# Optimization experiments

Hardware: AMD Instinct MI355X
Metric: run time of the kernel (lower is better)

## Reference

```python
import jax, jax.numpy as jnp
import numpy as np

B, D, DC, K = 65536, 768, 192, 100  # batch patterns, hidden_dim, codebook_hidden, num_clusters
LN_EPS = 1e-5


def setup_inputs() -> dict:
    key = jax.random.key(0)
    ks = jax.random.split(key, 12)
    w = lambda k, shape: (jax.random.normal(k, shape, jnp.float32) * 0.02)
    return {
        "hidden": jax.random.normal(ks[0], (B, D), jnp.float32),
        "W_low": w(ks[1], (DC, D)),   # nn.Linear(hidden_dim, codebook_hidden), torch (out,in)
        "b_low": jnp.zeros((DC,), jnp.float32),
        "ln_g": jnp.ones((DC,), jnp.float32),
        "ln_b": jnp.zeros((DC,), jnp.float32),
        "Wq": w(ks[2], (DC, DC)),
        "Wk": w(ks[3], (DC, DC)),
        "Wv": w(ks[4], (DC, DC)),
        "Wo": w(ks[5], (DC, DC)),
        "codebook": w(ks[6], (K, DC)),  # vp_codebook.weight
        "W_high": w(ks[7], (D, DC)),    # nn.Linear(codebook_hidden, hidden_dim)
        "b_high": jnp.zeros((D,), jnp.float32),
    }


def reference(hidden, W_low, b_low, ln_g, ln_b, Wq, Wk, Wv, Wo, codebook, W_high, b_high):
    # low projection: 768 -> 192
    pat = hidden @ W_low.T + b_low  # [B, DC]
    # LayerNorm over last dim
    mu = jnp.mean(pat, axis=-1, keepdims=True)
    var = jnp.mean(jnp.square(pat - mu), axis=-1, keepdims=True)
    pat = (pat - mu) * jax.lax.rsqrt(var + LN_EPS) * ln_g + ln_b
    # CrossAttention against codebook with NEGATED scores (distance-like)
    q = pat @ Wq.T            # [B, DC]
    k = codebook @ Wk.T       # [K, DC]
    v = codebook @ Wv.T       # [K, DC]
    scores = -(q @ k.T)       # [B, K]
    attn_w = jax.nn.softmax(scores, axis=-1)
    attn_out = (attn_w @ v) @ Wo.T  # [B, DC]
    # argmin over attention weights -> codebook selection + gather
    idx = jnp.argmin(attn_w, axis=-1)   # [B] int
    z_q = codebook[idx]                 # [B, DC]
    # high projection on both branches
    pat_h = attn_out @ W_high.T + b_high  # [B, D]
    zq_h = z_q @ W_high.T + b_high        # [B, D]
    # straight-through estimator: pat + (z_q - pat).detach()
    return pat_h + jax.lax.stop_gradient(zq_h - pat_h)
```

## Files before the change

kernel.cpp:

```cpp
#include <hip/hip_runtime.h>

#define NB    65536
#define DIN   768
#define DCB   192
#define KCL   100
#define NJ    112

#define OFF_S    0
#define OFF_CS   19200
#define OFF_U    19312
#define OFF_T    19424
#define OFF_ZH   19536
#define OFF_FLAG 96336
#define OFF_CNT  96337
#define OFF_MTH  96340
#define OFF_KTIL 96340
#define OFF_LIST 139348

#define MARGIN 1e-4f
#define MTSC   64.0f
#define SCINV  0.015625f

typedef __attribute__((ext_vector_type(8))) _Float16 half8;
typedef __attribute__((ext_vector_type(4))) float    f32x4;


__global__ void kA1(const float* __restrict__ cb, const float* __restrict__ Wk,
                    float* __restrict__ ktil, int* __restrict__ flag,
                    int* __restrict__ cnt) {
  __shared__ float cbrow[DCB];
  int j = blockIdx.x, i = threadIdx.x;
  if (j == 0 && i == 0) { *flag = 0; *cnt = 0; }
  cbrow[i] = cb[j*DCB + i];
  __syncthreads();
  const float4* wr = (const float4*)&Wk[(size_t)i * DCB];
  double s0 = 0.0, s1 = 0.0;
  #pragma unroll 4
  for (int m4 = 0; m4 < DCB/4; m4++) {
    float4 w = wr[m4];
    s0 += (double)w.x * (double)cbrow[m4*4+0] + (double)w.z * (double)cbrow[m4*4+2];
    s1 += (double)w.y * (double)cbrow[m4*4+1] + (double)w.w * (double)cbrow[m4*4+3];
  }
  ktil[j*DCB+i] = (float)(s0 + s1);
}

__global__ void kA2(const float* __restrict__ Wq, const float* __restrict__ ktil,
                    const float* __restrict__ ln_g, const float* __restrict__ ln_b,
                    const float* __restrict__ b_low,
                    float* __restrict__ S, float* __restrict__ csum,
                    float* __restrict__ tv, float* __restrict__ u,
                    int* __restrict__ flag) {
  __shared__ float krow[DCB];
  __shared__ double red[DCB];
  int j = blockIdx.x, c = threadIdx.x;
  krow[c] = ktil[j*DCB + c];
  __syncthreads();
  double a0 = 0.0, a1 = 0.0;
  #pragma unroll 4
  for (int i = 0; i < DCB; i += 2) {
    a0 += (double)Wq[i*DCB+c]     * (double)krow[i];
    a1 += (double)Wq[(i+1)*DCB+c] * (double)krow[i+1];
  }
  double a = a0 + a1;
  float Sv = ln_g[c] * (float)a;
  S[j*DCB+c] = Sv;

  red[c] = (double)Sv; __syncthreads();
  if (c == 0) {
    double p0=0,p1=0,p2=0,p3=0;
    for (int i = 0; i < DCB; i += 4) { p0+=red[i]; p1+=red[i+1]; p2+=red[i+2]; p3+=red[i+3]; }
    csum[j] = (float)(p0+p1+p2+p3);
  }
  __syncthreads();
  red[c] = (double)ln_b[c] * a; __syncthreads();
  if (c == 0) {
    double p0=0,p1=0,p2=0,p3=0;
    for (int i = 0; i < DCB; i += 4) { p0+=red[i]; p1+=red[i+1]; p2+=red[i+2]; p3+=red[i+3]; }
    float tf = (float)(p0+p1+p2+p3); tv[j] = tf;
    if (tf != 0.0f) atomicOr(flag, 1);
  }
  __syncthreads();
  red[c] = (double)b_low[c] * (double)Sv; __syncthreads();
  if (c == 0) {
    double p0=0,p1=0,p2=0,p3=0;
    for (int i = 0; i < DCB; i += 4) { p0+=red[i]; p1+=red[i+1]; p2+=red[i+2]; p3+=red[i+3]; }
    u[j] = (float)(p0+p1+p2+p3);
  }
  __syncthreads();
  if (j == 0) {
    red[c] = (double)b_low[c]; __syncthreads();
    if (c == 0) {
      double p0=0,p1=0,p2=0,p3=0;
      for (int i = 0; i < DCB; i += 4) { p0+=red[i]; p1+=red[i+1]; p2+=red[i+2]; p3+=red[i+3]; }
      u[KCL] = (float)((p0+p1+p2+p3) / (double)DCB);
      for (int p = KCL+1; p < NJ; p++) u[p] = 0.f;
      for (int p = KCL;   p < NJ; p++) { csum[p] = 0.f; tv[p] = 0.f; }
    }
  }
}

__global__ void kA3(const float* __restrict__ W_low, const float* __restrict__ S,
                    _Float16* __restrict__ Mth) {
  __shared__ float srow[DCB];
  int j = blockIdx.x / 3, st = blockIdx.x % 3;
  int t = threadIdx.x;
  int d = st * 256 + t;
  if (j < KCL && t < DCB) srow[t] = S[j*DCB + t];
  __syncthreads();
  float v;
  if (j < KCL) {
    double a = 0.0;
    for (int c = 0; c < DCB; c++) a += (double)W_low[(size_t)c*DIN + d] * (double)srow[c];
    v = (float)a;
  } else if (j == KCL) {
    double a = 0.0;
    for (int c = 0; c < DCB; c++) a += (double)W_low[(size_t)c*DIN + d];
    v = (float)(a / (double)DCB);
  } else {
    v = 0.f;
  }
  Mth[(size_t)j*DIN + d] = (_Float16)(v * MTSC);
}

__global__ void kA4(const float* __restrict__ cb, const float* __restrict__ W_high,
                    const float* __restrict__ b_high, float* __restrict__ ZH) {
  __shared__ float cbrow[DCB];
  int j = blockIdx.x, t = threadIdx.x;
  if (t < DCB) cbrow[t] = cb[j*DCB + t];
  __syncthreads();
  #pragma unroll
  for (int kd = 0; kd < 3; kd++) {
    int d = t + 256*kd;
    const float4* wr = (const float4*)&W_high[(size_t)d * DCB];
    double s0 = 0.0, s1 = 0.0;
    #pragma unroll 4
    for (int c4 = 0; c4 < DCB/4; c4++) {
      float4 w = wr[c4];
      s0 += (double)w.x * (double)cbrow[c4*4+0] + (double)w.z * (double)cbrow[c4*4+2];
      s1 += (double)w.y * (double)cbrow[c4*4+1] + (double)w.w * (double)cbrow[c4*4+3];
    }
    ZH[(size_t)j*DIN + d] = (float)(s0 + s1 + (double)b_high[d]);
  }
}

__global__ __launch_bounds__(256, 2)
void kB(const float* __restrict__ hidden, float* __restrict__ out,
        const _Float16* __restrict__ Mth, const float* __restrict__ u,
        const float* __restrict__ csum, const float* __restrict__ ZH,
        const int* __restrict__ flag, int* __restrict__ cnt,
        unsigned short* __restrict__ list,
        const float* __restrict__ S, const float* __restrict__ tv,
        const float* __restrict__ W_low, const float* __restrict__ b_low) {
  const int tid = threadIdx.x;
  __shared__ __align__(16) _Float16 Bs[2][14336];
  if (*flag == 0) {
    const int lane = tid & 63;
    const int wv   = tid >> 6;
    const int lj   = lane & 15, lk = lane >> 4;
    const int R    = blockIdx.x * 128 + wv * 32;

    char* BsB = (char*)&Bs[0][0];

    const char* srcp[7]; int dstp[7];
    #pragma unroll
    for (int i = 0; i < 7; i++) {
      int o    = ((wv*7 + i)*64 + lane) * 16;
      int row  = o >> 8;
      int colb = o & 255;
      srcp[i] = (const char*)Mth + row*1536 + colb;
      dstp[i] = row*256 + (colb ^ ((row & 7) << 4));
    }

    const float* A0 = hidden + (size_t)(R + lj) * DIN + lk * 8;
    const float* A1 = A0 + 16 * DIN;

    f32x4 acc[2][7];
    #pragma unroll
    for (int m = 0; m < 2; m++)
      #pragma unroll
      for (int nj = 0; nj < 7; nj++) acc[m][nj] = (f32x4){0.f, 0.f, 0.f, 0.f};

    uint4 stg[7];
    #pragma unroll
    for (int i = 0; i < 7; i++) stg[i] = *(const uint4*)(srcp[i]);
    float4 Ac[2][2];
    Ac[0][0] = *(const float4*)(A0); Ac[0][1] = *(const float4*)(A0 + 4);
    Ac[1][0] = *(const float4*)(A1); Ac[1][1] = *(const float4*)(A1 + 4);
    #pragma unroll
    for (int i = 0; i < 7; i++) *(uint4*)(BsB + dstp[i]) = stg[i];
    __syncthreads();

    for (int kc = 0; kc < 6; kc++) {
      const int cur = kc & 1;
      if (kc < 5) {
        #pragma unroll
        for (int i = 0; i < 7; i++)
          stg[i] = *(const uint4*)(srcp[i] + (kc + 1) * 256);
      }
      #pragma unroll
      for (int s = 0; s < 4; s++) {
        const int g = kc*4 + s;
        float4 An[2][2];
        if (g < 23) {
          const float* p0 = A0 + (g + 1) * 32;
          const float* p1 = A1 + (g + 1) * 32;
          An[0][0] = *(const float4*)(p0); An[0][1] = *(const float4*)(p0 + 4);
          An[1][0] = *(const float4*)(p1); An[1][1] = *(const float4*)(p1 + 4);
        }
        half8 bfr[7];
        const char* bbase = BsB + cur * 28672;
        #pragma unroll
        for (int nj = 0; nj < 7; nj++) {
          int row = nj*16 + lj;
          int off = row*256 + ((lk*16 + s*64) ^ ((row & 7) << 4));
          bfr[nj] = *(const half8*)(bbase + off);
        }
        #pragma unroll
        for (int m = 0; m < 2; m++) {
          half8 ah;
          ah[0] = (_Float16)Ac[m][0].x; ah[1] = (_Float16)Ac[m][0].y;
          ah[2] = (_Float16)Ac[m][0].z; ah[3] = (_Float16)Ac[m][0].w;
          ah[4] = (_Float16)Ac[m][1].x; ah[5] = (_Float16)Ac[m][1].y;
          ah[6] = (_Float16)Ac[m][1].z; ah[7] = (_Float16)Ac[m][1].w;
          #pragma unroll
          for (int nj = 0; nj < 7; nj++)
            acc[m][nj] = __builtin_amdgcn_mfma_f32_16x16x32_f16(ah, bfr[nj], acc[m][nj], 0, 0, 0);
        }
        if (g < 23) {
          Ac[0][0] = An[0][0]; Ac[0][1] = An[0][1];
          Ac[1][0] = An[1][0]; Ac[1][1] = An[1][1];
        }
      }
      if (kc < 5) {
        #pragma unroll
        for (int i = 0; i < 7; i++)
          *(uint4*)(BsB + (cur ^ 1) * 28672 + dstp[i]) = stg[i];
      }
      __syncthreads();
    }

    float uj[7], cj[7];
    #pragma unroll
    for (int nj = 0; nj < 7; nj++) { int j = nj*16 + lj; uj[nj] = u[j]; cj[nj] = csum[j]; }
    const float u100 = u[KCL];

    int idxr[2][4];
    #pragma unroll
    for (int m = 0; m < 2; m++) {
      #pragma unroll
      for (int r = 0; r < 4; r++) {
        float mu = __shfl(acc[m][6][r], (lane & 48) + 4, 64) * SCINV + u100;
        float b1 = -3.4e38f, b2 = -3.4e38f; int i1 = 0;
        #pragma unroll
        for (int nj = 0; nj < 7; nj++) {
          int j = nj*16 + lj;
          float sv = acc[m][nj][r] * SCINV + uj[nj] - mu * cj[nj];
          sv = (j < KCL) ? sv : -3.4e38f;
          if (sv > b1) { b2 = b1; b1 = sv; i1 = j; }
          else if (sv > b2) { b2 = sv; }
        }
        #pragma unroll
        for (int off = 1; off < 16; off <<= 1) {
          float ob1 = __shfl_xor(b1, off, 64);
          int   oi1 = __shfl_xor(i1, off, 64);
          float ob2 = __shfl_xor(b2, off, 64);
          if (ob1 > b1 || (ob1 == b1 && oi1 < i1)) {
            b2 = fmaxf(b1, fmaxf(b2, ob2)); b1 = ob1; i1 = oi1;
          } else {
            b2 = fmaxf(ob1, fmaxf(b2, ob2));
          }
        }
        idxr[m][r] = i1;
        if (lj == 0 && (b1 - b2) <= MARGIN) {
          int p = atomicAdd(cnt, 1);
          list[p] = (unsigned short)(R + m*16 + lk*4 + r);
        }
      }
    }

    #pragma unroll
    for (int rr = 0; rr < 32; rr++) {
      int idx = __shfl(idxr[rr >> 4][rr & 3], ((rr & 15) >> 2) << 4, 64);
      const float4* zs = (const float4*)(ZH + (size_t)idx * DIN);
      float4* od = (float4*)(out + (size_t)(R + rr) * DIN);
      od[lane]       = zs[lane];
      od[lane + 64]  = zs[lane + 64];
      od[lane + 128] = zs[lane + 128];
    }
  } else {
    __shared__ float hrow2[DIN];
    __shared__ float patv[DCB];
    __shared__ float redf[2];
    __shared__ float Gsc[KCL];
    __shared__ int   sidx;
    const int r0 = blockIdx.x * 128;
    for (int rr = 0; rr < 128; rr++) {
      const size_t row = (size_t)(r0 + rr);
      __syncthreads();
      for (int d = tid; d < DIN; d += 256) hrow2[d] = hidden[row * DIN + d];
      __syncthreads();
      if (tid < DCB) {
        float a = b_low[tid];
        for (int d = 0; d < DIN; d++) a += hrow2[d] * W_low[(size_t)tid * DIN + d];
        patv[tid] = a;
      }
      __syncthreads();
      if (tid == 0) {
        float mu = 0.f; for (int c = 0; c < DCB; c++) mu += patv[c]; mu /= (float)DCB;
        float var = 0.f; for (int c = 0; c < DCB; c++) { float dd = patv[c] - mu; var += dd * dd; }
        var /= (float)DCB;
        redf[0] = mu; redf[1] = rsqrtf(var + 1e-5f);
      }
      __syncthreads();
      if (tid < DCB) patv[tid] = (patv[tid] - redf[0]) * redf[1];
      __syncthreads();
      if (tid < KCL) {
        float s = tv[tid];
        for (int c = 0; c < DCB; c++) s += patv[c] * S[(size_t)tid * DCB + c];
        Gsc[tid] = s;
      }
      __syncthreads();
      if (tid == 0) {
        float best = -3.4e38f; int bi = 0;
        for (int j = 0; j < KCL; j++) if (Gsc[j] > best) { best = Gsc[j]; bi = j; }
        sidx = bi;
      }
      __syncthreads();
      {
        int idx = sidx;
        for (int d4 = tid; d4 < DIN / 4; d4 += 256) {
          float4 v = *(const float4*)&ZH[(size_t)idx * DIN + d4 * 4];
          *(float4*)&out[row * DIN + d4 * 4] = v;
        }
      }
    }
  }
}

__global__ void kC(const float* __restrict__ hidden, float* __restrict__ out,
                   const float* __restrict__ W_low, const float* __restrict__ b_low,
                   const float* __restrict__ S, const float* __restrict__ ZH,
                   const int* __restrict__ cnt, const unsigned short* __restrict__ list) {
  __shared__ float  hrow[DIN];
  __shared__ double pat[DCB];
  __shared__ double smu;
  __shared__ double sc[KCL];
  __shared__ int    bidx;
  const int n = *cnt;
  const int tid = threadIdx.x;
  for (int it = blockIdx.x; it < n; it += gridDim.x) {
    const int row = (int)list[it];
    __syncthreads();
    for (int d = tid; d < DIN; d += 256) hrow[d] = hidden[(size_t)row * DIN + d];
    __syncthreads();
    if (tid < DCB) {
      const float* wl = W_low + (size_t)tid * DIN;
      double a = (double)b_low[tid];
      for (int d = 0; d < DIN; d += 4) {
        a += (double)hrow[d]   * (double)wl[d]
           + (double)hrow[d+1] * (double)wl[d+1]
           + (double)hrow[d+2] * (double)wl[d+2]
           + (double)hrow[d+3] * (double)wl[d+3];
      }
      pat[tid] = a;
    }
    __syncthreads();
    if (tid == 0) {
      double m = 0.0;
      for (int c = 0; c < DCB; c++) m += pat[c];
      smu = m / (double)DCB;
    }
    __syncthreads();
    if (tid < KCL) {
      const float* sr = S + (size_t)tid * DCB;
      const double mu = smu;
      double a = 0.0;
      for (int c = 0; c < DCB; c++) a += (pat[c] - mu) * (double)sr[c];
      sc[tid] = a;
    }
    __syncthreads();
    if (tid == 0) {
      double best = -1e300; int bi = 0;
      for (int j = 0; j < KCL; j++)
        if (sc[j] > best) { best = sc[j]; bi = j; }
      bidx = bi;
    }
    __syncthreads();
    {
      const int idx = bidx;
      for (int d4 = tid; d4 < DIN / 4; d4 += 256) {
        float4 v = *(const float4*)(ZH + (size_t)idx * DIN + d4 * 4);
        *(float4*)(out + (size_t)row * DIN + d4 * 4) = v;
      }
    }
  }
}

extern "C" void kernel_launch(void* const* d_in, const int* in_sizes, int n_in,
                              void* d_out, int out_size, void* d_ws, size_t ws_size,
                              hipStream_t stream) {
  const float* hidden = (const float*)d_in[0];
  const float* W_low  = (const float*)d_in[1];
  const float* b_low  = (const float*)d_in[2];
  const float* ln_g   = (const float*)d_in[3];
  const float* ln_b   = (const float*)d_in[4];
  const float* Wq     = (const float*)d_in[5];
  const float* Wk     = (const float*)d_in[6];
  const float* cb     = (const float*)d_in[9];
  const float* W_high = (const float*)d_in[10];
  const float* b_high = (const float*)d_in[11];
  float* out = (float*)d_out;
  float* ws  = (float*)d_ws;

  float*          S    = ws + OFF_S;
  float*          csum = ws + OFF_CS;
  float*          u    = ws + OFF_U;
  float*          tv   = ws + OFF_T;
  float*          ZH   = ws + OFF_ZH;
  int*            flag = (int*)(ws + OFF_FLAG);
  int*            cnt  = (int*)(ws + OFF_CNT);
  _Float16*       Mth  = (_Float16*)(ws + OFF_MTH);
  float*          ktil = ws + OFF_KTIL;
  unsigned short* list = (unsigned short*)(ws + OFF_LIST);

  kA1<<<KCL, DCB, 0, stream>>>(cb, Wk, ktil, flag, cnt);
  kA2<<<KCL, DCB, 0, stream>>>(Wq, ktil, ln_g, ln_b, b_low, S, csum, tv, u, flag);
  kA3<<<NJ*3, 256, 0, stream>>>(W_low, S, Mth);
  kA4<<<KCL, 256, 0, stream>>>(cb, W_high, b_high, ZH);
  kB<<<NB / 128, 256, 0, stream>>>(hidden, out, Mth, u, csum, ZH, flag, cnt, list,
                                   S, tv, W_low, b_low);
  kC<<<2048, 256, 0, stream>>>(hidden, out, W_low, b_low, S, ZH, cnt, list);
}
```

Baseline: 577.7 us.

## Fuse precompute kernels into one launch and batch fallback rows in kC

Merges the four small precompute kernels (K projection, S/csum/u computation, Mth build, ZH build) into one kernel whose blocks take different roles, and zeroes the flag/count with a memset instead of doing it inside a kernel. This removes launch overhead and the serial dependencies between the small kernels. The fallback kernel kC now processes 8 listed rows per block, so each W_low and S value it loads is reused across 8 rows. The cost is more shared memory and registers per block, and a long serial chain inside the fused precompute blocks.

```diff
diff --git a/kernel.cpp b/kernel.cpp
--- a/kernel.cpp
+++ b/kernel.cpp
@@ -14,7 +14,6 @@
 #define OFF_FLAG 96336
 #define OFF_CNT  96337
 #define OFF_MTH  96340
-#define OFF_KTIL 96340
 #define OFF_LIST 139348
 
 #define MARGIN 1e-4f
@@ -24,122 +23,130 @@
 typedef __attribute__((ext_vector_type(8))) _Float16 half8;
 typedef __attribute__((ext_vector_type(4))) float    f32x4;
 
-
-__global__ void kA1(const float* __restrict__ cb, const float* __restrict__ Wk,
-                    float* __restrict__ ktil, int* __restrict__ flag,
-                    int* __restrict__ cnt) {
-  __shared__ float cbrow[DCB];
-  int j = blockIdx.x, i = threadIdx.x;
-  if (j == 0 && i == 0) { *flag = 0; *cnt = 0; }
-  cbrow[i] = cb[j*DCB + i];
-  __syncthreads();
-  const float4* wr = (const float4*)&Wk[(size_t)i * DCB];
-  double s0 = 0.0, s1 = 0.0;
-  #pragma unroll 4
-  for (int m4 = 0; m4 < DCB/4; m4++) {
-    float4 w = wr[m4];
-    s0 += (double)w.x * (double)cbrow[m4*4+0] + (double)w.z * (double)cbrow[m4*4+2];
-    s1 += (double)w.y * (double)cbrow[m4*4+1] + (double)w.w * (double)cbrow[m4*4+3];
-  }
-  ktil[j*DCB+i] = (float)(s0 + s1);
-}
-
-__global__ void kA2(const float* __restrict__ Wq, const float* __restrict__ ktil,
-                    const float* __restrict__ ln_g, const float* __restrict__ ln_b,
-                    const float* __restrict__ b_low,
-                    float* __restrict__ S, float* __restrict__ csum,
-                    float* __restrict__ tv, float* __restrict__ u,
-                    int* __restrict__ flag) {
-  __shared__ float krow[DCB];
-  __shared__ double red[DCB];
-  int j = blockIdx.x, c = threadIdx.x;
-  krow[c] = ktil[j*DCB + c];
-  __syncthreads();
-  double a0 = 0.0, a1 = 0.0;
-  #pragma unroll 4
-  for (int i = 0; i < DCB; i += 2) {
-    a0 += (double)Wq[i*DCB+c]     * (double)krow[i];
-    a1 += (double)Wq[(i+1)*DCB+c] * (double)krow[i+1];
-  }
-  double a = a0 + a1;
-  float Sv = ln_g[c] * (float)a;
-  S[j*DCB+c] = Sv;
-
-  red[c] = (double)Sv; __syncthreads();
-  if (c == 0) {
-    double p0=0,p1=0,p2=0,p3=0;
-    for (int i = 0; i < DCB; i += 4) { p0+=red[i]; p1+=red[i+1]; p2+=red[i+2]; p3+=red[i+3]; }
-    csum[j] = (float)(p0+p1+p2+p3);
-  }
-  __syncthreads();
-  red[c] = (double)ln_b[c] * a; __syncthreads();
-  if (c == 0) {
-    double p0=0,p1=0,p2=0,p3=0;
-    for (int i = 0; i < DCB; i += 4) { p0+=red[i]; p1+=red[i+1]; p2+=red[i+2]; p3+=red[i+3]; }
-    float tf = (float)(p0+p1+p2+p3); tv[j] = tf;
-    if (tf != 0.0f) atomicOr(flag, 1);
-  }
-  __syncthreads();
-  red[c] = (double)b_low[c] * (double)Sv; __syncthreads();
-  if (c == 0) {
-    double p0=0,p1=0,p2=0,p3=0;
-    for (int i = 0; i < DCB; i += 4) { p0+=red[i]; p1+=red[i+1]; p2+=red[i+2]; p3+=red[i+3]; }
-    u[j] = (float)(p0+p1+p2+p3);
-  }
-  __syncthreads();
-  if (j == 0) {
-    red[c] = (double)b_low[c]; __syncthreads();
-    if (c == 0) {
-      double p0=0,p1=0,p2=0,p3=0;
-      for (int i = 0; i < DCB; i += 4) { p0+=red[i]; p1+=red[i+1]; p2+=red[i+2]; p3+=red[i+3]; }
-      u[KCL] = (float)((p0+p1+p2+p3) / (double)DCB);
-      for (int p = KCL+1; p < NJ; p++) u[p] = 0.f;
-      for (int p = KCL;   p < NJ; p++) { csum[p] = 0.f; tv[p] = 0.f; }
-    }
-  }
-}
-
-__global__ void kA3(const float* __restrict__ W_low, const float* __restrict__ S,
-                    _Float16* __restrict__ Mth) {
-  __shared__ float srow[DCB];
-  int j = blockIdx.x / 3, st = blockIdx.x % 3;
-  int t = threadIdx.x;
-  int d = st * 256 + t;
-  if (j < KCL && t < DCB) srow[t] = S[j*DCB + t];
-  __syncthreads();
-  float v;
-  if (j < KCL) {
-    double a = 0.0;
-    for (int c = 0; c < DCB; c++) a += (double)W_low[(size_t)c*DIN + d] * (double)srow[c];
-    v = (float)a;
-  } else if (j == KCL) {
-    double a = 0.0;
-    for (int c = 0; c < DCB; c++) a += (double)W_low[(size_t)c*DIN + d];
-    v = (float)(a / (double)DCB);
+__global__ void kA(const float* __restrict__ cb, const float* __restrict__ Wk,
+                   const float* __restrict__ Wq, const float* __restrict__ ln_g,
+                   const float* __restrict__ ln_b, const float* __restrict__ b_low,
+                   const float* __restrict__ W_low, const float* __restrict__ W_high,
+                   const float* __restrict__ b_high,
+                   float* __restrict__ S, float* __restrict__ csum,
+                   float* __restrict__ tv, float* __restrict__ u,
+                   _Float16* __restrict__ Mth, float* __restrict__ ZH,
+                   int* __restrict__ flag) {
+  const int bj = blockIdx.x;
+  const int t  = threadIdx.x;
+  if (bj < NJ) {
+    __shared__ float  cbrow[DCB];
+    __shared__ float  krow[DCB];
+    __shared__ float  srow[DCB];
+    __shared__ double red[DCB];
+    const int j = bj;
+    if (j < KCL) {
+      if (t < DCB) cbrow[t] = cb[j*DCB + t];
+      __syncthreads();
+      if (t < DCB) {
+        const float4* wr = (const float4*)&Wk[(size_t)t * DCB];
+        double s0 = 0.0, s1 = 0.0;
+        #pragma unroll 4
+        for (int m4 = 0; m4 < DCB/4; m4++) {
+          float4 w = wr[m4];
+          s0 += (double)w.x * (double)cbrow[m4*4+0] + (double)w.z * (double)cbrow[m4*4+2];
+          s1 += (double)w.y * (double)cbrow[m4*4+1] + (double)w.w * (double)cbrow[m4*4+3];
+        }
+        krow[t] = (float)(s0 + s1);
+      }
+      __syncthreads();
+      double a = 0.0;
+      if (t < DCB) {
+        double a0 = 0.0, a1 = 0.0;
+        #pragma unroll 4
+        for (int i = 0; i < DCB; i += 2) {
+          a0 += (double)Wq[i*DCB+t]     * (double)krow[i];
+          a1 += (double)Wq[(i+1)*DCB+t] * (double)krow[i+1];
+        }
+        a = a0 + a1;
+        float Sv = ln_g[t] * (float)a;
+        srow[t] = Sv;
+        S[j*DCB + t] = Sv;
+      }
+      __syncthreads();
+      if (t < DCB) red[t] = (double)srow[t];
+      __syncthreads();
+      if (t == 0) {
+        double p0=0,p1=0,p2=0,p3=0;
+        for (int i = 0; i < DCB; i += 4) { p0+=red[i]; p1+=red[i+1]; p2+=red[i+2]; p3+=red[i+3]; }
+        csum[j] = (float)(p0+p1+p2+p3);
+      }
+      __syncthreads();
+      if (t < DCB) red[t] = (double)ln_b[t] * a;
+      __syncthreads();
+      if (t == 0) {
+        double p0=0,p1=0,p2=0,p3=0;
+        for (int i = 0; i < DCB; i += 4) { p0+=red[i]; p1+=red[i+1]; p2+=red[i+2]; p3+=red[i+3]; }
+        float tf = (float)(p0+p1+p2+p3); tv[j] = tf;
+        if (tf != 0.0f) atomicOr(flag, 1);
+      }
+      __syncthreads();
+      if (t < DCB) red[t] = (double)b_low[t] * (double)srow[t];
+      __syncthreads();
+      if (t == 0) {
+        double p0=0,p1=0,p2=0,p3=0;
+        for (int i = 0; i < DCB; i += 4) { p0+=red[i]; p1+=red[i+1]; p2+=red[i+2]; p3+=red[i+3]; }
+        u[j] = (float)(p0+p1+p2+p3);
+      }
+      __syncthreads();
+      if (j == 0) {
+        if (t < DCB) red[t] = (double)b_low[t];
+        __syncthreads();
+        if (t == 0) {
+          double p0=0,p1=0,p2=0,p3=0;
+          for (int i = 0; i < DCB; i += 4) { p0+=red[i]; p1+=red[i+1]; p2+=red[i+2]; p3+=red[i+3]; }
+          u[KCL] = (float)((p0+p1+p2+p3) / (double)DCB);
+          for (int p = KCL+1; p < NJ; p++) u[p] = 0.f;
+          for (int p = KCL;   p < NJ; p++) { csum[p] = 0.f; tv[p] = 0.f; }
+        }
+        __syncthreads();
+      }
+      #pragma unroll
+      for (int kd = 0; kd < 3; kd++) {
+        int d = t + 256*kd;
+        double a3 = 0.0;
+        for (int c = 0; c < DCB; c++)
+          a3 += (double)W_low[(size_t)c*DIN + d] * (double)srow[c];
+        Mth[(size_t)j*DIN + d] = (_Float16)(((float)a3) * MTSC);
+      }
+    } else if (j == KCL) {
+      #pragma unroll
+      for (int kd = 0; kd < 3; kd++) {
+        int d = t + 256*kd;
+        double a3 = 0.0;
+        for (int c = 0; c < DCB; c++) a3 += (double)W_low[(size_t)c*DIN + d];
+        Mth[(size_t)j*DIN + d] = (_Float16)(((float)(a3 / (double)DCB)) * MTSC);
+      }
+    } else {
+      #pragma unroll
+      for (int kd = 0; kd < 3; kd++) {
+        int d = t + 256*kd;
+        Mth[(size_t)j*DIN + d] = (_Float16)0.f;
+      }
+    }
   } else {
-    v = 0.f;
-  }
-  Mth[(size_t)j*DIN + d] = (_Float16)(v * MTSC);
-}
-
-__global__ void kA4(const float* __restrict__ cb, const float* __restrict__ W_high,
-                    const float* __restrict__ b_high, float* __restrict__ ZH) {
-  __shared__ float cbrow[DCB];
-  int j = blockIdx.x, t = threadIdx.x;
-  if (t < DCB) cbrow[t] = cb[j*DCB + t];
-  __syncthreads();
-  #pragma unroll
-  for (int kd = 0; kd < 3; kd++) {
-    int d = t + 256*kd;
-    const float4* wr = (const float4*)&W_high[(size_t)d * DCB];
-    double s0 = 0.0, s1 = 0.0;
-    #pragma unroll 4
-    for (int c4 = 0; c4 < DCB/4; c4++) {
-      float4 w = wr[c4];
-      s0 += (double)w.x * (double)cbrow[c4*4+0] + (double)w.z * (double)cbrow[c4*4+2];
-      s1 += (double)w.y * (double)cbrow[c4*4+1] + (double)w.w * (double)cbrow[c4*4+3];
-    }
-    ZH[(size_t)j*DIN + d] = (float)(s0 + s1 + (double)b_high[d]);
+    __shared__ float cbr2[DCB];
+    const int j2 = bj - NJ;
+    if (t < DCB) cbr2[t] = cb[j2*DCB + t];
+    __syncthreads();
+    #pragma unroll
+    for (int kd = 0; kd < 3; kd++) {
+      int d = t + 256*kd;
+      const float4* wr = (const float4*)&W_high[(size_t)d * DCB];
+      double s0 = 0.0, s1 = 0.0;
+      #pragma unroll 4
+      for (int c4 = 0; c4 < DCB/4; c4++) {
+        float4 w = wr[c4];
+        s0 += (double)w.x * (double)cbr2[c4*4+0] + (double)w.z * (double)cbr2[c4*4+2];
+        s1 += (double)w.y * (double)cbr2[c4*4+1] + (double)w.w * (double)cbr2[c4*4+3];
+      }
+      ZH[(size_t)j2*DIN + d] = (float)(s0 + s1 + (double)b_high[d]);
+    }
   }
 }
 
@@ -337,61 +344,79 @@
   }
 }
 
-__global__ void kC(const float* __restrict__ hidden, float* __restrict__ out,
-                   const float* __restrict__ W_low, const float* __restrict__ b_low,
-                   const float* __restrict__ S, const float* __restrict__ ZH,
-                   const int* __restrict__ cnt, const unsigned short* __restrict__ list) {
-  __shared__ float  hrow[DIN];
-  __shared__ double pat[DCB];
-  __shared__ double smu;
-  __shared__ double sc[KCL];
-  __shared__ int    bidx;
-  const int n = *cnt;
+__global__ __launch_bounds__(256)
+void kC(const float* __restrict__ hidden, float* __restrict__ out,
+        const float* __restrict__ W_low, const float* __restrict__ b_low,
+        const float* __restrict__ S, const float* __restrict__ ZH,
+        const int* __restrict__ cnt, const unsigned short* __restrict__ list) {
+  __shared__ float  hrow[8][DIN];
+  __shared__ double pat[8][DCB];
+  __shared__ double mu8[8];
+  __shared__ double sc[KCL][8];
+  __shared__ int    bidx[8];
   const int tid = threadIdx.x;
-  for (int it = blockIdx.x; it < n; it += gridDim.x) {
-    const int row = (int)list[it];
-    __syncthreads();
-    for (int d = tid; d < DIN; d += 256) hrow[d] = hidden[(size_t)row * DIN + d];
+  int n = *cnt; if (n > NB) n = NB;
+  const int nb = (n + 7) >> 3;
+  for (int bt = blockIdx.x; bt < nb; bt += gridDim.x) {
+    const int base = bt * 8;
+    const int cr = (n - base < 8) ? (n - base) : 8;
+    __syncthreads();
+    for (int f = tid; f < cr * 192; f += 256) {
+      int r = f / 192, d4 = f - r * 192;
+      ((float4*)&hrow[r][0])[d4] =
+        *(const float4*)&hidden[(size_t)list[base + r] * DIN + d4 * 4];
+    }
     __syncthreads();
     if (tid < DCB) {
-      const float* wl = W_low + (size_t)tid * DIN;
-      double a = (double)b_low[tid];
-      for (int d = 0; d < DIN; d += 4) {
-        a += (double)hrow[d]   * (double)wl[d]
-           + (double)hrow[d+1] * (double)wl[d+1]
-           + (double)hrow[d+2] * (double)wl[d+2]
-           + (double)hrow[d+3] * (double)wl[d+3];
-      }
-      pat[tid] = a;
-    }
-    __syncthreads();
-    if (tid == 0) {
+      const float4* wl = (const float4*)&W_low[(size_t)tid * DIN];
+      double a[8];
+      #pragma unroll
+      for (int r = 0; r < 8; r++) a[r] = (double)b_low[tid];
+      for (int d4 = 0; d4 < DIN/4; d4++) {
+        float4 w = wl[d4];
+        #pragma unroll
+        for (int r = 0; r < 8; r++) {
+          a[r] += (double)hrow[r][d4*4+0] * (double)w.x
+                + (double)hrow[r][d4*4+1] * (double)w.y
+                + (double)hrow[r][d4*4+2] * (double)w.z
+                + (double)hrow[r][d4*4+3] * (double)w.w;
+        }
+      }
+      #pragma unroll
+      for (int r = 0; r < 8; r++) pat[r][tid] = a[r];
+    }
+    __syncthreads();
+    if (tid < 8) {
       double m = 0.0;
-      for (int c = 0; c < DCB; c++) m += pat[c];
-      smu = m / (double)DCB;
+      for (int c = 0; c < DCB; c++) m += pat[tid][c];
+      mu8[tid] = m / (double)DCB;
     }
     __syncthreads();
     if (tid < KCL) {
       const float* sr = S + (size_t)tid * DCB;
-      const double mu = smu;
-      double a = 0.0;
-      for (int c = 0; c < DCB; c++) a += (pat[c] - mu) * (double)sr[c];
-      sc[tid] = a;
-    }
-    __syncthreads();
-    if (tid == 0) {
+      double a[8];
+      #pragma unroll
+      for (int r = 0; r < 8; r++) a[r] = 0.0;
+      for (int c = 0; c < DCB; c++) {
+        double sv = (double)sr[c];
+        #pragma unroll
+        for (int r = 0; r < 8; r++) a[r] += (pat[r][c] - mu8[r]) * sv;
+      }
+      #pragma unroll
+      for (int r = 0; r < 8; r++) sc[tid][r] = a[r];
+    }
+    __syncthreads();
+    if (tid < cr) {
       double best = -1e300; int bi = 0;
-      for (int j = 0; j < KCL; j++)
-        if (sc[j] > best) { best = sc[j]; bi = j; }
-      bidx = bi;
-    }
-    __syncthreads();
-    {
-      const int idx = bidx;
-      for (int d4 = tid; d4 < DIN / 4; d4 += 256) {
-        float4 v = *(const float4*)(ZH + (size_t)idx * DIN + d4 * 4);
-        *(float4*)(out + (size_t)row * DIN + d4 * 4) = v;
-      }
+      for (int jj = 0; jj < KCL; jj++)
+        if (sc[jj][tid] > best) { best = sc[jj][tid]; bi = jj; }
+      bidx[tid] = bi;
+    }
+    __syncthreads();
+    for (int f = tid; f < cr * 192; f += 256) {
+      int r = f / 192, d4 = f - r * 192;
+      float4 v = ((const float4*)&ZH[(size_t)bidx[r] * DIN])[d4];
+      ((float4*)&out[(size_t)list[base + r] * DIN])[d4] = v;
     }
   }
 }
@@ -420,13 +445,11 @@
   int*            flag = (int*)(ws + OFF_FLAG);
   int*            cnt  = (int*)(ws + OFF_CNT);
   _Float16*       Mth  = (_Float16*)(ws + OFF_MTH);
-  float*          ktil = ws + OFF_KTIL;
   unsigned short* list = (unsigned short*)(ws + OFF_LIST);
 
-  kA1<<<KCL, DCB, 0, stream>>>(cb, Wk, ktil, flag, cnt);
-  kA2<<<KCL, DCB, 0, stream>>>(Wq, ktil, ln_g, ln_b, b_low, S, csum, tv, u, flag);
-  kA3<<<NJ*3, 256, 0, stream>>>(W_low, S, Mth);
-  kA4<<<KCL, 256, 0, stream>>>(cb, W_high, b_high, ZH);
+  hipMemsetAsync((void*)flag, 0, 8, stream);
+  kA<<<NJ + KCL, 256, 0, stream>>>(cb, Wk, Wq, ln_g, ln_b, b_low, W_low, W_high,
+                                   b_high, S, csum, tv, u, Mth, ZH, flag);
   kB<<<NB / 128, 256, 0, stream>>>(hidden, out, Mth, u, csum, ZH, flag, cnt, list,
                                    S, tv, W_low, b_low);
   kC<<<2048, 256, 0, stream>>>(hidden, out, W_low, b_low, S, ZH, cnt, list);
```

Measured after the change: 507.0 us. -12.2%, faster.
